# Kernel tuning notes

Hardware: AMD Instinct MI355X
Metric: run time of the kernel (lower is better)

Reference implementation:

```python
import jax, jax.numpy as jnp
import numpy as np

N, H, W = 16, 60, 60
CIN, HID = 256, 10
# chain adjacency over 6 parts; torch.nonzero row-major order
EDGES = [(0,1),(1,0),(1,2),(2,1),(2,3),(3,2),(3,4),(4,3),(4,5),(5,4)]
PLL = [[1],[0,2],[1,3],[2,4],[3,5],[4]]  # part_list_list[v] = list of source parts u
EPS = 1e-5


def conv1x1(x, w, b=None):
    # x: [n,c,h,w], w: [o,c] -> [n,o,h,w]
    y = jnp.einsum('oc,nchw->nohw', w, x)
    return y if b is None else y + b[None, :, None, None]


def bn(x, g, b):
    # eval-mode InPlaceABN(activation='none'): running_mean=0, running_var=1
    s = (g * (1.0 / np.sqrt(1.0 + EPS))).astype(x.dtype)
    return x * s[None, :, None, None] + b[None, :, None, None]


def block2(x, c1w, c1g, c1b, c2w, c2g, c2b):
    # Conv1x1(no bias)+BN+ReLU -> Conv1x1(no bias)+BN+ReLU
    h = jax.nn.relu(bn(conv1x1(x, c1w), c1g, c1b))
    return jax.nn.relu(bn(conv1x1(h, c2w), c2g, c2b))


def setup_inputs():
    ks = iter(jax.random.split(jax.random.key(0), 64))
    def nrm(shape, s=1.0):
        return jax.random.normal(next(ks), shape, jnp.float32) * s
    D = {}
    for name in ['xf', 'xh0', 'xh1', 'xp0', 'xp1', 'xp2', 'xp3', 'xp4', 'xp5']:
        D[name] = nrm((N, HID, H, W))
    D['xp'] = nrm((N, CIN, H, W))
    # Dep_Context.project (live path) for each of 6 parts
    D['proj1_w'] = nrm((6, CIN, CIN), 0.05); D['proj1_g'] = 1.0 + nrm((6, CIN), 0.1); D['proj1_b'] = nrm((6, CIN), 0.1)
    D['proj2_w'] = nrm((6, 2*HID, CIN), 0.05); D['proj2_g'] = 1.0 + nrm((6, 2*HID), 0.1); D['proj2_b'] = nrm((6, 2*HID), 0.1)
    # Contexture att convs (out-channels vary per part: pad to 3, slice at use)
    D['att_w'] = nrm((6, 3, HID), 0.1); D['att_b'] = nrm((6, 3), 0.1)
    # grouped (groups=2) context att convs: [part, out(2), in_per_group(10)]
    D['ctx_w'] = nrm((6, 2, HID), 0.1); D['ctx_b'] = nrm((6, 2), 0.1)
    # Decomposition att convs (upper: 4 parts -> 5 ch; lower: 2 parts -> 3 ch)
    D['du_att_w'] = nrm((5, HID), 0.1); D['du_att_b'] = nrm((5,), 0.1)
    D['dl_att_w'] = nrm((3, HID), 0.1); D['dl_att_b'] = nrm((3,), 0.1)
    # 2-layer conv blocks: idx 0 = upper decomp, 1 = lower decomp, 2 = shared Part_Dependency
    D['blk_c1_w'] = nrm((3, 2*HID, 2*HID), 0.1); D['blk_c1_g'] = 1.0 + nrm((3, 2*HID), 0.1); D['blk_c1_b'] = nrm((3, 2*HID), 0.1)
    D['blk_c2_w'] = nrm((3, HID, 2*HID), 0.1); D['blk_c2_g'] = 1.0 + nrm((3, HID), 0.1); D['blk_c2_b'] = nrm((3, HID), 0.1)
    # per-node ConvGRU (1x1 kernels)
    D['gru_gate_w'] = nrm((6, 2*HID, 2*HID), 0.1); D['gru_gate_b'] = nrm((6, 2*HID), 0.1)
    D['gru_cand_w'] = nrm((6, HID, 2*HID), 0.1); D['gru_cand_b'] = nrm((6, HID), 0.1)
    return D


def _forward(xf, xh0, xh1, xp0, xp1, xp2, xp3, xp4, xp5, xp,
             proj1_w, proj1_g, proj1_b, proj2_w, proj2_g, proj2_b,
             att_w, att_b, ctx_w, ctx_b,
             du_att_w, du_att_b, dl_att_w, dl_att_b,
             blk_c1_w, blk_c1_g, blk_c1_b, blk_c2_w, blk_c2_g, blk_c2_b,
             gru_gate_w, gru_gate_b, gru_cand_w, gru_cand_b):
    xp_list = [xp0, xp1, xp2, xp3, xp4, xp5]
    # ---- Contexture / Dep_Context. NOTE: the original's coord-feature bmm
    # attention (query @ W @ node, softmax, bmm with p_fea) is DEAD CODE:
    # `co_context = p_fea` overwrites its result, so outputs only depend on
    # project(p_fea). We faithfully implement the live path.
    F_dep, att_soft, att_raw, ctx_att = [], [], [], []
    for i in range(6):
        h1 = jax.nn.relu(bn(conv1x1(xp, proj1_w[i]), proj1_g[i], proj1_b[i]))
        ctx = jax.nn.relu(bn(conv1x1(h1, proj2_w[i]), proj2_g[i], proj2_b[i]))  # [n,2*HID,h,w]
        fd = ctx[:, HID:]  # co_context half
        c = len(PLL[i]) + 1
        a = conv1x1(fd, att_w[i, :c], att_b[i, :c])
        att_raw.append(a)
        att_soft.append(jax.nn.softmax(a, axis=1))
        # grouped (groups=2) 1x1 conv over the 2*HID context
        o0 = conv1x1(ctx[:, :HID], ctx_w[i, 0:1], ctx_b[i, 0:1])
        o1 = conv1x1(ctx[:, HID:], ctx_w[i, 1:2], ctx_b[i, 1:2])
        ctx_att.append(jnp.concatenate([o0, o1], axis=1))
        F_dep.append(fd)
    # ---- Decomposition: upper half -> parts 1-4, lower half -> parts 5-6
    pu_map = conv1x1(xh0, du_att_w, du_att_b)
    pu_att = jax.nn.softmax(pu_map, axis=1)
    dec_pu = [block2(jnp.concatenate([xh0 * pu_att[:, j+1:j+2], xp_list[j]], axis=1),
                     blk_c1_w[0], blk_c1_g[0], blk_c1_b[0], blk_c2_w[0], blk_c2_g[0], blk_c2_b[0])
              for j in range(4)]
    pl_map = conv1x1(xh1, dl_att_w, dl_att_b)
    pl_att = jax.nn.softmax(pl_map, axis=1)
    dec_pl = [block2(jnp.concatenate([xh1 * pl_att[:, j+1:j+2], xp_list[4 + j]], axis=1),
                     blk_c1_w[1], blk_c1_g[1], blk_c1_b[1], blk_c2_w[1], blk_c2_g[1], blk_c2_b[1])
              for j in range(2)]
    # ---- Part_Dependency messages along graph edges (shared weights)
    xpp = [[] for _ in range(6)]
    for (u, v) in EDGES:
        k = 1 + PLL[u].index(v)
        m_in = jnp.concatenate([att_soft[u][:, k:k+1] * F_dep[u], xp_list[v]], axis=1)
        xpp[v].append(block2(m_in, blk_c1_w[2], blk_c1_g[2], blk_c1_b[2],
                             blk_c2_w[2], blk_c2_g[2], blk_c2_b[2]))
    # ---- per-node ConvGRU update (1x1 kernel, one step; h = xp_list[i])
    xp_new = []
    for i in range(6):
        msg = (dec_pu[i] if i < 4 else dec_pl[i - 4]) + sum(xpp[i])
        h = xp_list[i]
        gates = conv1x1(jnp.concatenate([msg, h], axis=1), gru_gate_w[i], gru_gate_b[i])
        r = jax.nn.sigmoid(gates[:, :HID])
        z = jax.nn.sigmoid(gates[:, HID:])
        cand = jnp.tanh(conv1x1(jnp.concatenate([msg, r * h], axis=1), gru_cand_w[i], gru_cand_b[i]))
        xp_new.append((1.0 - z) * h + z * cand)
    return (jnp.concatenate(xp_new, axis=1),      # [n,60,h,w] xp_list_new
            pu_map,                                # [n,5,h,w]
            pl_map,                                # [n,3,h,w]
            jnp.concatenate(att_raw, axis=1),      # [n,16,h,w] Fdep_att_list
            jnp.concatenate(ctx_att, axis=1))      # [n,12,h,w] context_att_list


def reference(xf, xh0, xh1, xp0, xp1, xp2, xp3, xp4, xp5, xp,
              proj1_w, proj1_g, proj1_b, proj2_w, proj2_g, proj2_b,
              att_w, att_b, ctx_w, ctx_b,
              du_att_w, du_att_b, dl_att_w, dl_att_b,
              blk_c1_w, blk_c1_g, blk_c1_b, blk_c2_w, blk_c2_g, blk_c2_b,
              gru_gate_w, gru_gate_b, gru_cand_w, gru_cand_b):
    return _forward(xf, xh0, xh1, xp0, xp1, xp2, xp3, xp4, xp5, xp,
                    proj1_w, proj1_g, proj1_b, proj2_w, proj2_g, proj2_b,
                    att_w, att_b, ctx_w, ctx_b,
                    du_att_w, du_att_b, dl_att_w, dl_att_b,
                    blk_c1_w, blk_c1_g, blk_c1_b, blk_c2_w, blk_c2_g, blk_c2_b,
                    gru_gate_w, gru_gate_b, gru_cand_w, gru_cand_b)
```

## Files before the change

### kernel.cpp

```cpp
#include <hip/hip_runtime.h>


#define P_TOT 57600
#define RSQEPS 0.99999500003749969f
#define O2 3456000
#define O3 3744000
#define O4 3916800
#define O5 4838400

typedef __attribute__((ext_vector_type(8))) short s8v;
typedef __attribute__((ext_vector_type(4))) short s4v;
typedef __attribute__((ext_vector_type(4))) float f4v;

__device__ __forceinline__ float bf2f(short s) {
  union { unsigned int i; float f; } u;
  u.i = ((unsigned int)(unsigned short)s) << 16;
  return u.f;
}
__device__ __forceinline__ short f2bf(float f) {
  union { float f; unsigned int i; } u; u.f = f;
  unsigned int r = (u.i + 0x7FFFu + ((u.i >> 16) & 1u)) >> 16;
  return (short)r;
}

__device__ __forceinline__ int swz(int m, int c) {
  return m * 256 + (c ^ ((((m >> 3) ^ m) & 7) << 3));
}

__device__ __forceinline__ void fence() {
  asm volatile("" ::: "memory");
  __builtin_amdgcn_sched_barrier(0);
}

#define NW1U 49152
#define NUW  55296
__global__ __launch_bounds__(256) void k0_prep(
    const float* __restrict__ w1, const float* __restrict__ w2,
    short* __restrict__ w1p, short* __restrict__ w2p) {
  int i = blockIdx.x * 256 + threadIdx.x;
  if (i < NW1U) {
    int g = i;
    int lane = g & 63, t1 = g >> 6;
    int kk = t1 & 7, t2 = t1 >> 3;
    int ni = t2 & 3, t3 = t2 >> 2;
    int nblk = t3 & 3, head = t3 >> 2;
    int o = nblk * 64 + ni * 16 + (lane & 15);
    const float* src = w1 + (size_t)head * 65536 + (size_t)o * 256 + kk * 32 + (lane >> 4) * 8;
    short* d = w1p + (size_t)g * 8;
#pragma unroll
    for (int j = 0; j < 8; ++j) d[j] = f2bf(src[j]);
  } else {
    int g = i - NW1U;
    int lane = g & 63, t1 = g >> 6;
    int kk = t1 & 7, t2 = t1 >> 3;
    int f = t2 & 1, head = t2 >> 1;
    int row = f * 16 + (lane & 15);
    short* d = w2p + (size_t)g * 8;
    if (row < 20) {
      const float* src = w2 + (size_t)head * 5120 + (size_t)row * 256 + kk * 32 + (lane >> 4) * 8;
#pragma unroll
      for (int j = 0; j < 8; ++j) d[j] = f2bf(src[j]);
    } else {
#pragma unroll
      for (int j = 0; j < 8; ++j) d[j] = 0;
    }
  }
}

__global__ __launch_bounds__(256, 3) void k1_proj(
    const float* __restrict__ xp, const short* __restrict__ w1p,
    const float* __restrict__ g1, const float* __restrict__ b1,
    const short* __restrict__ w2p,
    const float* __restrict__ g2, const float* __restrict__ b2,
    short* __restrict__ ctx) {
  __shared__ __align__(16) short sA[48 * 256];
  __shared__ __align__(16) short sH[48 * 256];
  const int t = threadIdx.x;
  const int p0 = blockIdx.x * 48;
  const int n = p0 / 3600;
  const int hw0 = p0 % 3600;
  const int lane = t & 63;
  const int wid = t >> 6;
  const int l15 = lane & 15;
  const int lg = lane >> 4;

  const float* xpn = xp + (size_t)n * 256 * 3600 + hw0;
#pragma unroll
  for (int it = 0; it < 6; ++it) {
    int u = it * 256 + t;
    int q = u % 6;
    int c = u / 6;
    int m0 = q * 8;
    const float* src = xpn + c * 3600 + m0;
    f4v v0 = *((const f4v*)src);
    f4v v1 = *((const f4v*)(src + 4));
#pragma unroll
    for (int j = 0; j < 4; ++j) {
      sA[swz(m0 + j, c)] = f2bf(v0[j]);
      sA[swz(m0 + 4 + j, c)] = f2bf(v1[j]);
    }
  }
  __syncthreads();

  for (int head = 0; head < 6; ++head) {
    f4v acc[4][3];
#pragma unroll
    for (int mi = 0; mi < 4; ++mi)
#pragma unroll
      for (int nf = 0; nf < 3; ++nf) acc[mi][nf] = (f4v){0.f, 0.f, 0.f, 0.f};
    const int n0 = wid * 64;
    const short* wb = w1p + (size_t)(head * 4 + wid) * (4 * 8 * 64 * 8);
    s8v aWa[4], aWb[4];
#pragma unroll
    for (int mi = 0; mi < 4; ++mi)
      aWa[mi] = *((const s8v*)(wb + ((mi * 8 + 0) * 64 + lane) * 8));
#pragma unroll
    for (int kk = 0; kk < 8; ++kk) {
      s8v (&cur)[4] = (kk & 1) ? aWb : aWa;
      s8v (&nxt)[4] = (kk & 1) ? aWa : aWb;
      if (kk < 7) {
#pragma unroll
        for (int mi = 0; mi < 4; ++mi)
          nxt[mi] = *((const s8v*)(wb + ((mi * 8 + kk + 1) * 64 + lane) * 8));
      }
      s8v bP[3];
#pragma unroll
      for (int nf = 0; nf < 3; ++nf)
        bP[nf] = *((const s8v*)&sA[swz(nf * 16 + l15, kk * 32 + lg * 8)]);
#pragma unroll
      for (int mi = 0; mi < 4; ++mi)
#pragma unroll
        for (int nf = 0; nf < 3; ++nf)
          acc[mi][nf] = __builtin_amdgcn_mfma_f32_16x16x32_bf16(cur[mi], bP[nf], acc[mi][nf], 0, 0, 0);
    }
#pragma unroll
    for (int mi = 0; mi < 4; ++mi) {
      int o4 = n0 + mi * 16 + lg * 4;
      f4v s4 = *((const f4v*)(g1 + head * 256 + o4));
      f4v c4 = *((const f4v*)(b1 + head * 256 + o4));
#pragma unroll
      for (int nf = 0; nf < 3; ++nf) {
        int pix = nf * 16 + l15;
        s4v pk;
#pragma unroll
        for (int r = 0; r < 4; ++r)
          pk[r] = f2bf(fmaxf(acc[mi][nf][r] * (s4[r] * RSQEPS) + c4[r], 0.f));
        *((s4v*)&sH[swz(pix, o4)]) = pk;
      }
    }
    __syncthreads();
    if (wid < 3) {
      f4v a20 = {0.f, 0.f, 0.f, 0.f}, a21 = {0.f, 0.f, 0.f, 0.f};
#pragma unroll
      for (int kk = 0; kk < 8; ++kk) {
        s8v bH = *((const s8v*)&sH[swz(wid * 16 + l15, kk * 32 + lg * 8)]);
        s8v w20 = *((const s8v*)(w2p + ((size_t)(((head * 2 + 0) * 8 + kk) * 64 + lane)) * 8));
        s8v w21 = *((const s8v*)(w2p + ((size_t)(((head * 2 + 1) * 8 + kk) * 64 + lane)) * 8));
        a20 = __builtin_amdgcn_mfma_f32_16x16x32_bf16(w20, bH, a20, 0, 0, 0);
        a21 = __builtin_amdgcn_mfma_f32_16x16x32_bf16(w21, bH, a21, 0, 0, 0);
      }
#pragma unroll
      for (int mf = 0; mf < 2; ++mf) {
        int ch4 = mf * 16 + lg * 4;
        if (ch4 < 20) {
          f4v s4 = *((const f4v*)(g2 + head * 20 + ch4));
          f4v c4 = *((const f4v*)(b2 + head * 20 + ch4));
          f4v& aa = mf ? a21 : a20;
#pragma unroll
          for (int r = 0; r < 4; ++r) {
            float v = fmaxf(aa[r] * (s4[r] * RSQEPS) + c4[r], 0.f);
            ctx[(size_t)(head * 20 + ch4 + r) * P_TOT + p0 + wid * 16 + l15] = f2bf(v);
          }
        }
      }
    }
    __syncthreads();
  }
}

__global__ __launch_bounds__(256) void k2_att(
    const short* __restrict__ ctx,
    const float* __restrict__ attw, const float* __restrict__ attb,
    const float* __restrict__ ctxw, const float* __restrict__ ctxb,
    float* __restrict__ ws_att, float* __restrict__ out) {
  int p = blockIdx.x * 256 + threadIdx.x;
  const int i = blockIdx.y;
  int n = p / 3600, hw = p % 3600;
  const int att_off[6] = {0, 2, 5, 8, 11, 14};
  float fd[10], c0[10];
#pragma unroll
  for (int c = 0; c < 10; ++c) {
    c0[c] = bf2f(ctx[(size_t)(i * 20 + c) * P_TOT + p]);
    fd[c] = bf2f(ctx[(size_t)(i * 20 + 10 + c) * P_TOT + p]);
  }
  const int ci = (i == 0 || i == 5) ? 2 : 3;
  float a[3];
#pragma unroll
  for (int j = 0; j < 3; ++j) {
    if (j < ci) {
      float s = attb[i * 3 + j];
#pragma unroll
      for (int c = 0; c < 10; ++c) s += attw[(i * 3 + j) * 10 + c] * fd[c];
      a[j] = s;
      out[O4 + ((size_t)n * 16 + att_off[i] + j) * 3600 + hw] = s;
    }
  }
  float mx = fmaxf(a[0], a[1]);
  if (ci == 3) mx = fmaxf(mx, a[2]);
  float se = 0.f;
#pragma unroll
  for (int j = 0; j < 3; ++j)
    if (j < ci) { a[j] = __expf(a[j] - mx); se += a[j]; }
  float inv = 1.f / se;
#pragma unroll
  for (int j = 0; j < 3; ++j)
    if (j < ci) ws_att[(size_t)(i * 3 + j) * P_TOT + p] = a[j] * inv;
  float o0 = ctxb[i * 2 + 0];
  float o1 = ctxb[i * 2 + 1];
#pragma unroll
  for (int c = 0; c < 10; ++c) {
    o0 += ctxw[(i * 2 + 0) * 10 + c] * c0[c];
    o1 += ctxw[(i * 2 + 1) * 10 + c] * fd[c];
  }
  out[O5 + ((size_t)n * 12 + i * 2 + 0) * 3600 + hw] = o0;
  out[O5 + ((size_t)n * 12 + i * 2 + 1) * 3600 + hw] = o1;
}

__global__ __launch_bounds__(256) void k3_gates(
    const float* __restrict__ xh0, const float* __restrict__ xh1,
    const float* __restrict__ duw, const float* __restrict__ dub,
    const float* __restrict__ dlw, const float* __restrict__ dlb,
    float* __restrict__ ws_pu, float* __restrict__ ws_pl, float* __restrict__ out) {
  int p = blockIdx.x * 256 + threadIdx.x;
  int n = p / 3600, hw = p % 3600;
  if (blockIdx.y == 0) {
    float h[10];
#pragma unroll
    for (int c = 0; c < 10; ++c) h[c] = xh0[((size_t)n * 10 + c) * 3600 + hw];
    float a[5];
#pragma unroll
    for (int j = 0; j < 5; ++j) {
      float s = dub[j];
#pragma unroll
      for (int c = 0; c < 10; ++c) s += duw[j * 10 + c] * h[c];
      a[j] = s;
      out[O2 + ((size_t)n * 5 + j) * 3600 + hw] = s;
    }
    float mx = a[0];
#pragma unroll
    for (int j = 1; j < 5; ++j) mx = fmaxf(mx, a[j]);
    float se = 0.f;
#pragma unroll
    for (int j = 0; j < 5; ++j) { a[j] = __expf(a[j] - mx); se += a[j]; }
    float inv = 1.f / se;
#pragma unroll
    for (int j = 0; j < 5; ++j) ws_pu[(size_t)j * P_TOT + p] = a[j] * inv;
  } else {
    float h[10];
#pragma unroll
    for (int c = 0; c < 10; ++c) h[c] = xh1[((size_t)n * 10 + c) * 3600 + hw];
    float b3[3];
#pragma unroll
    for (int j = 0; j < 3; ++j) {
      float s = dlb[j];
#pragma unroll
      for (int c = 0; c < 10; ++c) s += dlw[j * 10 + c] * h[c];
      b3[j] = s;
      out[O3 + ((size_t)n * 3 + j) * 3600 + hw] = s;
    }
    float mx = fmaxf(fmaxf(b3[0], b3[1]), b3[2]);
    float se = 0.f;
#pragma unroll
    for (int j = 0; j < 3; ++j) { b3[j] = __expf(b3[j] - mx); se += b3[j]; }
    float inv = 1.f / se;
#pragma unroll
    for (int j = 0; j < 3; ++j) ws_pl[(size_t)j * P_TOT + p] = b3[j] * inv;
  }
}

static __device__ const int INC_N[6] = {1, 2, 2, 2, 2, 1};
static __device__ const int INC_U[6][2] = {{1, 0}, {0, 2}, {1, 3}, {2, 4}, {3, 5}, {4, 0}};
static __device__ const int INC_K[6][2] = {{1, 0}, {1, 1}, {2, 1}, {2, 1}, {2, 1}, {2, 0}};

template <bool ACCUM>
__device__ __forceinline__ void block2_l2(
    const float* __restrict__ w1, const float* __restrict__ s1, const float* __restrict__ b1,
    const float* __restrict__ w2, const float* __restrict__ s2, const float* __restrict__ b2,
    const float* __restrict__ inaA, const float* __restrict__ inbA,
    const float* __restrict__ inaB, const float* __restrict__ inbB,
    float* __restrict__ outA, float* __restrict__ outB) {
  float hA[20], hB[20];
#pragma unroll
  for (int o = 0; o < 20; ++o) {
    float aA = 0.f, aB = 0.f;
#pragma unroll
    for (int c = 0; c < 10; ++c) {
      float wlo = w1[o * 20 + c], whi = w1[o * 20 + 10 + c];
      aA += wlo * inaA[c] + whi * inbA[c];
      aB += wlo * inaB[c] + whi * inbB[c];
    }
    float ss = s1[o], bb = b1[o];
    hA[o] = fmaxf(aA * ss + bb, 0.f);
    hB[o] = fmaxf(aB * ss + bb, 0.f);
    if ((o & 3) == 3) fence();
  }
#pragma unroll
  for (int o = 0; o < 10; ++o) {
    float aA = 0.f, aB = 0.f;
#pragma unroll
    for (int c = 0; c < 20; ++c) {
      float w = w2[o * 20 + c];
      aA += w * hA[c];
      aB += w * hB[c];
    }
    float ss = s2[o], bb = b2[o];
    float vA = fmaxf(aA * ss + bb, 0.f);
    float vB = fmaxf(aB * ss + bb, 0.f);
    if (ACCUM) { outA[o] += vA; outB[o] += vB; }
    else       { outA[o] = vA;  outB[o] = vB; }
    if ((o & 3) == 3) fence();
  }
  fence();
}

__global__ __launch_bounds__(256) void k4a_msg(
    const float* __restrict__ xh0, const float* __restrict__ xh1,
    const float* __restrict__ xp0, const float* __restrict__ xp1,
    const float* __restrict__ xp2, const float* __restrict__ xp3,
    const float* __restrict__ xp4, const float* __restrict__ xp5,
    const float* __restrict__ ws_pu, const float* __restrict__ ws_pl,
    const float* __restrict__ ws_att, const short* __restrict__ ctx,
    const float* __restrict__ c1wg, const float* __restrict__ c1gg, const float* __restrict__ c1bg,
    const float* __restrict__ c2wg, const float* __restrict__ c2gg, const float* __restrict__ c2bg,
    float* __restrict__ ws_msg) {
  __shared__ float W[1980];
  const int t = threadIdx.x;
  const int node = blockIdx.y;
  for (int u = t; u < 1980; u += 256) {
    float v;
    if (u < 1200) v = c1wg[u];
    else if (u < 1260) v = c1gg[u - 1200] * RSQEPS;
    else if (u < 1320) v = c1bg[u - 1260];
    else if (u < 1920) v = c2wg[u - 1320];
    else if (u < 1950) v = c2gg[u - 1920] * RSQEPS;
    else v = c2bg[u - 1950];
    W[u] = v;
  }
  __syncthreads();
  const int sdec = (node < 4) ? 0 : 1;
  const int pA = blockIdx.x * 512 + t;
  const bool vB = pA + 256 < P_TOT;
  const int pB = vB ? pA + 256 : P_TOT - 1;
  const int nA = pA / 3600, hwA = pA % 3600;
  const int nB = pB / 3600, hwB = pB % 3600;
  const float* xhp = (node < 4) ? xh0 : xh1;
  const float* xpl = node == 0 ? xp0 : node == 1 ? xp1 : node == 2 ? xp2
                   : node == 3 ? xp3 : node == 4 ? xp4 : xp5;
  float xpiA[10], xpiB[10];
#pragma unroll
  for (int c = 0; c < 10; ++c) {
    xpiA[c] = xpl[((size_t)nA * 10 + c) * 3600 + hwA];
    xpiB[c] = xpl[((size_t)nB * 10 + c) * 3600 + hwB];
  }
  const float* gatep = (node < 4) ? ws_pu : ws_pl;
  const int gidx = (node < 4) ? node + 1 : node - 3;
  float attgA = gatep[(size_t)gidx * P_TOT + pA];
  float attgB = gatep[(size_t)gidx * P_TOT + pB];
  float gatedA[10], gatedB[10], msgA[10], msgB[10];
#pragma unroll
  for (int c = 0; c < 10; ++c) {
    gatedA[c] = xhp[((size_t)nA * 10 + c) * 3600 + hwA] * attgA;
    gatedB[c] = xhp[((size_t)nB * 10 + c) * 3600 + hwB] * attgB;
  }
  fence();
  block2_l2<false>(W + sdec * 400, W + 1200 + sdec * 20, W + 1260 + sdec * 20,
                   W + 1320 + sdec * 200, W + 1920 + sdec * 10, W + 1950 + sdec * 10,
                   gatedA, xpiA, gatedB, xpiB, msgA, msgB);
  const int ne = INC_N[node];
#pragma unroll 1
  for (int e = 0; e < ne; ++e) {
    int uu = INC_U[node][e], kk = INC_K[node][e];
    float avA = ws_att[(size_t)(uu * 3 + kk) * P_TOT + pA];
    float avB = ws_att[(size_t)(uu * 3 + kk) * P_TOT + pB];
#pragma unroll
    for (int c = 0; c < 10; ++c) {
      gatedA[c] = avA * bf2f(ctx[(size_t)(uu * 20 + 10 + c) * P_TOT + pA]);
      gatedB[c] = avB * bf2f(ctx[(size_t)(uu * 20 + 10 + c) * P_TOT + pB]);
    }
    fence();
    block2_l2<true>(W + 800, W + 1240, W + 1300, W + 1720, W + 1940, W + 1970,
                    gatedA, xpiA, gatedB, xpiB, msgA, msgB);
  }
#pragma unroll
  for (int c = 0; c < 10; ++c) {
    ws_msg[(size_t)(node * 10 + c) * P_TOT + pA] = msgA[c];
    if (vB) ws_msg[(size_t)(node * 10 + c) * P_TOT + pB] = msgB[c];
  }
}

__global__ __launch_bounds__(256) void k4b_gru(
    const float* __restrict__ xp0, const float* __restrict__ xp1,
    const float* __restrict__ xp2, const float* __restrict__ xp3,
    const float* __restrict__ xp4, const float* __restrict__ xp5,
    const float* __restrict__ ws_msg,
    const float* __restrict__ gwg, const float* __restrict__ gbg,
    const float* __restrict__ cwg, const float* __restrict__ cbg,
    float* __restrict__ out) {
  __shared__ float W[630];
  const int t = threadIdx.x;
  const int node = blockIdx.y;
  for (int u = t; u < 630; u += 256) {
    float v;
    if (u < 400) v = gwg[node * 400 + u];
    else if (u < 420) v = gbg[node * 20 + (u - 400)];
    else if (u < 620) v = cwg[node * 200 + (u - 420)];
    else v = cbg[node * 10 + (u - 620)];
    W[u] = v;
  }
  __syncthreads();
  const int pA = blockIdx.x * 512 + t;
  const bool vB = pA + 256 < P_TOT;
  const int pB = vB ? pA + 256 : P_TOT - 1;
  const int nA = pA / 3600, hwA = pA % 3600;
  const int nB = pB / 3600, hwB = pB % 3600;
  const float* xpl = node == 0 ? xp0 : node == 1 ? xp1 : node == 2 ? xp2
                   : node == 3 ? xp3 : node == 4 ? xp4 : xp5;
  float xpiA[10], xpiB[10], msgA[10], msgB[10];
#pragma unroll
  for (int c = 0; c < 10; ++c) {
    xpiA[c] = xpl[((size_t)nA * 10 + c) * 3600 + hwA];
    xpiB[c] = xpl[((size_t)nB * 10 + c) * 3600 + hwB];
    msgA[c] = ws_msg[(size_t)(node * 10 + c) * P_TOT + pA];
    msgB[c] = ws_msg[(size_t)(node * 10 + c) * P_TOT + pB];
  }
  fence();
  float g20A[20], g20B[20];
#pragma unroll
  for (int o = 0; o < 20; ++o) {
    float aA = W[400 + o], aB = aA;
#pragma unroll
    for (int c = 0; c < 10; ++c) {
      float wlo = W[o * 20 + c], whi = W[o * 20 + 10 + c];
      aA += wlo * msgA[c] + whi * xpiA[c];
      aB += wlo * msgB[c] + whi * xpiB[c];
    }
    g20A[o] = aA; g20B[o] = aB;
    if ((o & 3) == 3) fence();
  }
  float rhA[10], rhB[10];
#pragma unroll
  for (int c = 0; c < 10; ++c) {
    rhA[c] = xpiA[c] / (1.f + __expf(-g20A[c]));
    rhB[c] = xpiB[c] / (1.f + __expf(-g20B[c]));
  }
#pragma unroll
  for (int o = 0; o < 10; ++o) {
    float aA = W[620 + o], aB = aA;
#pragma unroll
    for (int c = 0; c < 10; ++c) {
      float wlo = W[420 + o * 20 + c], whi = W[420 + o * 20 + 10 + c];
      aA += wlo * msgA[c] + whi * rhA[c];
      aB += wlo * msgB[c] + whi * rhB[c];
    }
    float cdA = 1.f - 2.f / (__expf(2.f * aA) + 1.f);
    float cdB = 1.f - 2.f / (__expf(2.f * aB) + 1.f);
    float zA = 1.f / (1.f + __expf(-g20A[10 + o]));
    float zB = 1.f / (1.f + __expf(-g20B[10 + o]));
    out[((size_t)nA * 60 + node * 10 + o) * 3600 + hwA] = (1.f - zA) * xpiA[o] + zA * cdA;
    if (vB)
      out[((size_t)nB * 60 + node * 10 + o) * 3600 + hwB] = (1.f - zB) * xpiB[o] + zB * cdB;
    if ((o & 3) == 3) fence();
  }
}

extern "C" void kernel_launch(void* const* d_in, const int* in_sizes, int n_in,
                              void* d_out, int out_size, void* d_ws, size_t ws_size,
                              hipStream_t stream) {
  const float* xh0 = (const float*)d_in[1];
  const float* xh1 = (const float*)d_in[2];
  const float* xp0 = (const float*)d_in[3];
  const float* xp1 = (const float*)d_in[4];
  const float* xp2 = (const float*)d_in[5];
  const float* xp3 = (const float*)d_in[6];
  const float* xp4 = (const float*)d_in[7];
  const float* xp5 = (const float*)d_in[8];
  const float* xp  = (const float*)d_in[9];
  const float* p1w = (const float*)d_in[10];
  const float* p1g = (const float*)d_in[11];
  const float* p1b = (const float*)d_in[12];
  const float* p2w = (const float*)d_in[13];
  const float* p2g = (const float*)d_in[14];
  const float* p2b = (const float*)d_in[15];
  const float* attw = (const float*)d_in[16];
  const float* attb = (const float*)d_in[17];
  const float* ctxw = (const float*)d_in[18];
  const float* ctxb = (const float*)d_in[19];
  const float* duw = (const float*)d_in[20];
  const float* dub = (const float*)d_in[21];
  const float* dlw = (const float*)d_in[22];
  const float* dlb = (const float*)d_in[23];
  const float* c1w = (const float*)d_in[24];
  const float* c1g = (const float*)d_in[25];
  const float* c1b = (const float*)d_in[26];
  const float* c2w = (const float*)d_in[27];
  const float* c2g = (const float*)d_in[28];
  const float* c2b = (const float*)d_in[29];
  const float* gw  = (const float*)d_in[30];
  const float* gb  = (const float*)d_in[31];
  const float* cw  = (const float*)d_in[32];
  const float* cb  = (const float*)d_in[33];

  char* wsb = (char*)d_ws;
  short* w1p   = (short*)(wsb);
  short* w2p   = (short*)(wsb + 786432);
  short* ctxb2 = (short*)(wsb + 884736);
  float* ws_att = (float*)(wsb + 14708736);
  float* ws_pu  = (float*)(wsb + 18855936);
  float* ws_pl  = (float*)(wsb + 20007936);
  float* ws_msg = (float*)(wsb + 20699136);
  float* out = (float*)d_out;

  k0_prep<<<216, 256, 0, stream>>>(p1w, p2w, w1p, w2p);
  k1_proj<<<1200, 256, 0, stream>>>(xp, w1p, p1g, p1b, w2p, p2g, p2b, ctxb2);
  k2_att<<<dim3(225, 6), 256, 0, stream>>>(ctxb2, attw, attb, ctxw, ctxb, ws_att, out);
  k3_gates<<<dim3(225, 2), 256, 0, stream>>>(xh0, xh1, duw, dub, dlw, dlb, ws_pu, ws_pl, out);
  k4a_msg<<<dim3(113, 6), 256, 0, stream>>>(xh0, xh1, xp0, xp1, xp2, xp3, xp4, xp5,
      ws_pu, ws_pl, ws_att, ctxb2, c1w, c1g, c1b, c2w, c2g, c2b, ws_msg);
  k4b_gru<<<dim3(113, 6), 256, 0, stream>>>(xp0, xp1, xp2, xp3, xp4, xp5,
      ws_msg, gw, gb, cw, cb, out);
}
```

Measured before the change: 174.3 us.

## Process two pixel tiles per block in projection kernel to reuse weight registers

Each block of the projection kernel now loads two 48-pixel input tiles into double shared memory and handles both per head. For each head the full first-layer weight fragment set (4x8 bf16 vectors) is loaded into registers once and reused across both tiles, halving weight global loads. The grid is halved to 600 blocks and the occupancy hint is dropped. The trade-off is higher register pressure from holding 32 vector fragments, larger shared memory per block, and fewer blocks to spread over CUs.

```diff
diff --git a/kernel.cpp b/kernel.cpp
--- a/kernel.cpp
+++ b/kernel.cpp
@@ -67,114 +67,117 @@
   }
 }
 
-__global__ __launch_bounds__(256, 3) void k1_proj(
+__global__ __launch_bounds__(256) void k1_proj(
     const float* __restrict__ xp, const short* __restrict__ w1p,
     const float* __restrict__ g1, const float* __restrict__ b1,
     const short* __restrict__ w2p,
     const float* __restrict__ g2, const float* __restrict__ b2,
     short* __restrict__ ctx) {
-  __shared__ __align__(16) short sA[48 * 256];
+  __shared__ __align__(16) short sA[2][48 * 256];
   __shared__ __align__(16) short sH[48 * 256];
   const int t = threadIdx.x;
-  const int p0 = blockIdx.x * 48;
-  const int n = p0 / 3600;
-  const int hw0 = p0 % 3600;
   const int lane = t & 63;
   const int wid = t >> 6;
   const int l15 = lane & 15;
   const int lg = lane >> 4;
 
-  const float* xpn = xp + (size_t)n * 256 * 3600 + hw0;
-#pragma unroll
-  for (int it = 0; it < 6; ++it) {
-    int u = it * 256 + t;
-    int q = u % 6;
-    int c = u / 6;
-    int m0 = q * 8;
-    const float* src = xpn + c * 3600 + m0;
-    f4v v0 = *((const f4v*)src);
-    f4v v1 = *((const f4v*)(src + 4));
-#pragma unroll
-    for (int j = 0; j < 4; ++j) {
-      sA[swz(m0 + j, c)] = f2bf(v0[j]);
-      sA[swz(m0 + 4 + j, c)] = f2bf(v1[j]);
+#pragma unroll
+  for (int tile = 0; tile < 2; ++tile) {
+    int tt = blockIdx.x * 2 + tile;
+    int n = tt / 75;
+    int hw0 = (tt % 75) * 48;
+    const float* xpn = xp + (size_t)n * 256 * 3600 + hw0;
+#pragma unroll
+    for (int it = 0; it < 6; ++it) {
+      int u = it * 256 + t;
+      int q = u % 6;
+      int c = u / 6;
+      int m0 = q * 8;
+      const float* src = xpn + c * 3600 + m0;
+      f4v v0 = *((const f4v*)src);
+      f4v v1 = *((const f4v*)(src + 4));
+#pragma unroll
+      for (int j = 0; j < 4; ++j) {
+        sA[tile][swz(m0 + j, c)] = f2bf(v0[j]);
+        sA[tile][swz(m0 + 4 + j, c)] = f2bf(v1[j]);
+      }
     }
   }
   __syncthreads();
 
   for (int head = 0; head < 6; ++head) {
-    f4v acc[4][3];
-#pragma unroll
-    for (int mi = 0; mi < 4; ++mi)
-#pragma unroll
-      for (int nf = 0; nf < 3; ++nf) acc[mi][nf] = (f4v){0.f, 0.f, 0.f, 0.f};
     const int n0 = wid * 64;
     const short* wb = w1p + (size_t)(head * 4 + wid) * (4 * 8 * 64 * 8);
-    s8v aWa[4], aWb[4];
+    s8v wf[4][8];
 #pragma unroll
     for (int mi = 0; mi < 4; ++mi)
-      aWa[mi] = *((const s8v*)(wb + ((mi * 8 + 0) * 64 + lane) * 8));
-#pragma unroll
-    for (int kk = 0; kk < 8; ++kk) {
-      s8v (&cur)[4] = (kk & 1) ? aWb : aWa;
-      s8v (&nxt)[4] = (kk & 1) ? aWa : aWb;
-      if (kk < 7) {
+#pragma unroll
+      for (int kk = 0; kk < 8; ++kk)
+        wf[mi][kk] = *((const s8v*)(wb + ((size_t)(mi * 8 + kk) * 64 + lane) * 8));
+
+#pragma unroll 1
+    for (int tile = 0; tile < 2; ++tile) {
+      const int p0 = (blockIdx.x * 2 + tile) * 48;
+      f4v acc[4][3];
+#pragma unroll
+      for (int mi = 0; mi < 4; ++mi)
+#pragma unroll
+        for (int nf = 0; nf < 3; ++nf) acc[mi][nf] = (f4v){0.f, 0.f, 0.f, 0.f};
+#pragma unroll
+      for (int kk = 0; kk < 8; ++kk) {
+        s8v bP[3];
+#pragma unroll
+        for (int nf = 0; nf < 3; ++nf)
+          bP[nf] = *((const s8v*)&sA[tile][swz(nf * 16 + l15, kk * 32 + lg * 8)]);
 #pragma unroll
         for (int mi = 0; mi < 4; ++mi)
-          nxt[mi] = *((const s8v*)(wb + ((mi * 8 + kk + 1) * 64 + lane) * 8));
+#pragma unroll
+          for (int nf = 0; nf < 3; ++nf)
+            acc[mi][nf] = __builtin_amdgcn_mfma_f32_16x16x32_bf16(wf[mi][kk], bP[nf], acc[mi][nf], 0, 0, 0);
       }
-      s8v bP[3];
-#pragma unroll
-      for (int nf = 0; nf < 3; ++nf)
-        bP[nf] = *((const s8v*)&sA[swz(nf * 16 + l15, kk * 32 + lg * 8)]);
-#pragma unroll
-      for (int mi = 0; mi < 4; ++mi)
-#pragma unroll
-        for (int nf = 0; nf < 3; ++nf)
-          acc[mi][nf] = __builtin_amdgcn_mfma_f32_16x16x32_bf16(cur[mi], bP[nf], acc[mi][nf], 0, 0, 0);
-    }
-#pragma unroll
-    for (int mi = 0; mi < 4; ++mi) {
-      int o4 = n0 + mi * 16 + lg * 4;
-      f4v s4 = *((const f4v*)(g1 + head * 256 + o4));
-      f4v c4 = *((const f4v*)(b1 + head * 256 + o4));
-#pragma unroll
-      for (int nf = 0; nf < 3; ++nf) {
-        int pix = nf * 16 + l15;
-        s4v pk;
-#pragma unroll
-        for (int r = 0; r < 4; ++r)
-          pk[r] = f2bf(fmaxf(acc[mi][nf][r] * (s4[r] * RSQEPS) + c4[r], 0.f));
-        *((s4v*)&sH[swz(pix, o4)]) = pk;
+#pragma unroll
+      for (int mi = 0; mi < 4; ++mi) {
+        int o4 = n0 + mi * 16 + lg * 4;
+        f4v s4 = *((const f4v*)(g1 + head * 256 + o4));
+        f4v c4 = *((const f4v*)(b1 + head * 256 + o4));
+#pragma unroll
+        for (int nf = 0; nf < 3; ++nf) {
+          int pix = nf * 16 + l15;
+          s4v pk;
+#pragma unroll
+          for (int r = 0; r < 4; ++r)
+            pk[r] = f2bf(fmaxf(acc[mi][nf][r] * (s4[r] * RSQEPS) + c4[r], 0.f));
+          *((s4v*)&sH[swz(pix, o4)]) = pk;
+        }
       }
-    }
-    __syncthreads();
-    if (wid < 3) {
-      f4v a20 = {0.f, 0.f, 0.f, 0.f}, a21 = {0.f, 0.f, 0.f, 0.f};
-#pragma unroll
-      for (int kk = 0; kk < 8; ++kk) {
-        s8v bH = *((const s8v*)&sH[swz(wid * 16 + l15, kk * 32 + lg * 8)]);
-        s8v w20 = *((const s8v*)(w2p + ((size_t)(((head * 2 + 0) * 8 + kk) * 64 + lane)) * 8));
-        s8v w21 = *((const s8v*)(w2p + ((size_t)(((head * 2 + 1) * 8 + kk) * 64 + lane)) * 8));
-        a20 = __builtin_amdgcn_mfma_f32_16x16x32_bf16(w20, bH, a20, 0, 0, 0);
-        a21 = __builtin_amdgcn_mfma_f32_16x16x32_bf16(w21, bH, a21, 0, 0, 0);
-      }
-#pragma unroll
-      for (int mf = 0; mf < 2; ++mf) {
-        int ch4 = mf * 16 + lg * 4;
-        if (ch4 < 20) {
-          f4v s4 = *((const f4v*)(g2 + head * 20 + ch4));
-          f4v c4 = *((const f4v*)(b2 + head * 20 + ch4));
-          f4v& aa = mf ? a21 : a20;
-#pragma unroll
-          for (int r = 0; r < 4; ++r) {
-            float v = fmaxf(aa[r] * (s4[r] * RSQEPS) + c4[r], 0.f);
-            ctx[(size_t)(head * 20 + ch4 + r) * P_TOT + p0 + wid * 16 + l15] = f2bf(v);
+      __syncthreads();
+      if (wid < 3) {
+        f4v a20 = {0.f, 0.f, 0.f, 0.f}, a21 = {0.f, 0.f, 0.f, 0.f};
+#pragma unroll
+        for (int kk = 0; kk < 8; ++kk) {
+          s8v bH = *((const s8v*)&sH[swz(wid * 16 + l15, kk * 32 + lg * 8)]);
+          s8v w20 = *((const s8v*)(w2p + ((size_t)(((head * 2 + 0) * 8 + kk) * 64 + lane)) * 8));
+          s8v w21 = *((const s8v*)(w2p + ((size_t)(((head * 2 + 1) * 8 + kk) * 64 + lane)) * 8));
+          a20 = __builtin_amdgcn_mfma_f32_16x16x32_bf16(w20, bH, a20, 0, 0, 0);
+          a21 = __builtin_amdgcn_mfma_f32_16x16x32_bf16(w21, bH, a21, 0, 0, 0);
+        }
+#pragma unroll
+        for (int mf = 0; mf < 2; ++mf) {
+          int ch4 = mf * 16 + lg * 4;
+          if (ch4 < 20) {
+            f4v s4 = *((const f4v*)(g2 + head * 20 + ch4));
+            f4v c4 = *((const f4v*)(b2 + head * 20 + ch4));
+            f4v& aa = mf ? a21 : a20;
+#pragma unroll
+            for (int r = 0; r < 4; ++r) {
+              float v = fmaxf(aa[r] * (s4[r] * RSQEPS) + c4[r], 0.f);
+              ctx[(size_t)(head * 20 + ch4 + r) * P_TOT + p0 + wid * 16 + l15] = f2bf(v);
+            }
           }
         }
       }
-    }
-    __syncthreads();
+      __syncthreads();
+    }
   }
 }
 
@@ -521,7 +524,7 @@
   float* out = (float*)d_out;
 
   k0_prep<<<216, 256, 0, stream>>>(p1w, p2w, w1p, w2p);
-  k1_proj<<<1200, 256, 0, stream>>>(xp, w1p, p1g, p1b, w2p, p2g, p2b, ctxb2);
+  k1_proj<<<600, 256, 0, stream>>>(xp, w1p, p1g, p1b, w2p, p2g, p2b, ctxb2);
   k2_att<<<dim3(225, 6), 256, 0, stream>>>(ctxb2, attw, attb, ctxw, ctxb, ws_att, out);
   k3_gates<<<dim3(225, 2), 256, 0, stream>>>(xh0, xh1, duw, dub, dlw, dlb, ws_pu, ws_pl, out);
   k4a_msg<<<dim3(113, 6), 256, 0, stream>>>(xh0, xh1, xp0, xp1, xp2, xp3, xp4, xp5,
```

Result: slower. 256.7 us (+47.3%).
